# Kernel optimization log

Hardware: AMD Instinct MI355X
Metric: run time of the kernel (lower is better)

The kernel has to match this reference:

```python
import jax, jax.numpy as jnp
import numpy as np

B, T, F = 128, 64, 2048
N, H, C = 1024, 1024, 22  # neurons, hidden_size, num_classes


def setup_inputs() -> dict:
    key = jax.random.key(0)
    ks = jax.random.split(key, 9)
    def w(k, shape, fan_in):
        return jax.random.normal(k, shape, dtype=jnp.float32) / np.sqrt(fan_in)
    return {
        "x": jax.random.normal(ks[0], (B, T, F), dtype=jnp.float32),
        "W1": w(ks[1], (N, F), F),
        "b1": jnp.zeros((N,), jnp.float32),
        "W_ih": w(ks[2], (4 * H, N), N),
        "b_ih": jnp.zeros((4 * H,), jnp.float32),
        "W_hh": w(ks[3], (4 * H, H), H),
        "b_hh": jnp.zeros((4 * H,), jnp.float32),
        "Wc": w(ks[4], (C, H), H),
        "bc": jnp.zeros((C,), jnp.float32),
    }


def reference(x, W1, b1, W_ih, b_ih, W_hh, b_hh, Wc, bc):
    b, t, _ = x.shape
    h0 = jnp.zeros((b, H), x.dtype)
    c0 = jnp.zeros((b, H), x.dtype)
    # Precompute the input-side projections for every step (batched GEMMs):
    z = jax.nn.relu(jnp.einsum("btf,nf->btn", x, W1) + b1)        # [B,T,N]
    xg = jnp.einsum("btn,gn->btg", z, W_ih) + b_ih                 # [B,T,4H]

    def step(carry, xg_t):
        h, c = carry
        gates = xg_t + h @ W_hh.T + b_hh                           # [B,4H]
        i, f, g, o = jnp.split(gates, 4, axis=-1)                  # torch LSTMCell gate order
        c = jax.nn.sigmoid(f) * c + jax.nn.sigmoid(i) * jnp.tanh(g)
        h = jax.nn.sigmoid(o) * jnp.tanh(c)
        return (h, c), h

    _, hs = jax.lax.scan(step, (h0, c0), jnp.swapaxes(xg, 0, 1))    # hs: [T,B,H]
    scores = jnp.einsum("tbh,ch->tbc", hs, Wc) + bc                # [T,B,C]
    scores = jnp.swapaxes(scores, 0, 1).reshape(-1, Wc.shape[0])    # [B*T, C]
    return scores
```

## Files before the change

### kernel.cpp

```cpp
#include <hip/hip_runtime.h>
#include <hip/hip_bf16.h>

typedef short bf16x8 __attribute__((ext_vector_type(8)));
typedef float f32x4 __attribute__((ext_vector_type(4)));

#define B_ 128
#define T_ 64
#define F_ 2048
#define N_ 1024
#define H_ 1024
#define C_ 22

__device__ __forceinline__ ushort f2bf(float f) {
    union { float f; unsigned u; } v; v.f = f;
    unsigned u = v.u;
    unsigned r = (u + 0x7FFFu + ((u >> 16) & 1u)) >> 16;
    return (ushort)r;
}
__device__ __forceinline__ float bf2f(ushort h) {
    union { unsigned u; float f; } v; v.u = ((unsigned)h) << 16;
    return v.f;
}

__global__ __launch_bounds__(256) void cvt_f32_bf16(const float* __restrict__ in,
                                                    ushort* __restrict__ out, int n4) {
    int i = blockIdx.x * blockDim.x + threadIdx.x;
    if (i < n4) {
        float4 v = ((const float4*)in)[i];
        ushort4 o;
        o.x = f2bf(v.x); o.y = f2bf(v.y); o.z = f2bf(v.z); o.w = f2bf(v.w);
        ((ushort4*)out)[i] = o;
    }
}

__global__ __launch_bounds__(256) void cvt_wc(const float* __restrict__ Wc,
                                              ushort* __restrict__ Wcb) {
    int i = blockIdx.x * 256 + threadIdx.x;
    int row = i >> 10;
    Wcb[i] = (row < C_) ? f2bf(Wc[i]) : (ushort)0;
}

__device__ __forceinline__ void gload16(const void* g, void* l) {
    __builtin_amdgcn_global_load_lds(
        (const __attribute__((address_space(1))) unsigned int*)g,
        (__attribute__((address_space(3))) unsigned int*)l, 16, 0, 0);
}

template<int K, bool RELU>
__global__ __launch_bounds__(256) void gemm_bt(const ushort* __restrict__ A,
                                               const ushort* __restrict__ Bm,
                                               const float* __restrict__ bias1,
                                               const float* __restrict__ bias2,
                                               ushort* __restrict__ C,
                                               int Nt, int Nn) {
    __shared__ ushort sA[128 * 32];
    __shared__ ushort sB[128 * 32];
    const int tid = threadIdx.x;
    const int lane = tid & 63, wv = tid >> 6;
    const int tm = blockIdx.x / Nt, tn = blockIdx.x % Nt;
    const int wm = wv >> 1, wn = wv & 1;

    const ushort* gA = A + (size_t)(tm * 128 + (tid >> 2)) * K + (tid & 3) * 8;
    const ushort* gB = Bm + (size_t)(tn * 128 + (tid >> 2)) * K + (tid & 3) * 8;
    char* lAb = (char*)sA + wv * 1024;
    char* lBb = (char*)sB + wv * 1024;

    f32x4 acc[4][4] = {};

    for (int kt = 0; kt < K / 32; kt++) {
        const ushort* a0 = gA + kt * 32;
        const ushort* b0 = gB + kt * 32;
        gload16(a0, lAb);
        gload16(a0 + 64 * K, lAb + 4096);
        gload16(b0, lBb);
        gload16(b0 + 64 * K, lBb + 4096);
        __syncthreads();

        bf16x8 af[4], bfv[4];
#pragma unroll
        for (int i = 0; i < 4; i++)
            af[i] = *(const bf16x8*)&sA[(wm * 64 + i * 16 + (lane & 15)) * 32 + (lane >> 4) * 8];
#pragma unroll
        for (int j = 0; j < 4; j++)
            bfv[j] = *(const bf16x8*)&sB[(wn * 64 + j * 16 + (lane & 15)) * 32 + (lane >> 4) * 8];
#pragma unroll
        for (int i = 0; i < 4; i++)
#pragma unroll
            for (int j = 0; j < 4; j++)
                acc[i][j] = __builtin_amdgcn_mfma_f32_16x16x32_bf16(af[i], bfv[j], acc[i][j], 0, 0, 0);
        __syncthreads();
    }

#pragma unroll
    for (int j = 0; j < 4; j++) {
        int n = tn * 128 + wn * 64 + j * 16 + (lane & 15);
        float bias = bias1[n] + (bias2 ? bias2[n] : 0.f);
#pragma unroll
        for (int i = 0; i < 4; i++) {
            int mbase = tm * 128 + wm * 64 + i * 16 + (lane >> 4) * 4;
#pragma unroll
            for (int r = 0; r < 4; r++) {
                float v = acc[i][j][r] + bias;
                if (RELU) v = v > 0.f ? v : 0.f;
                C[(size_t)(mbase + r) * Nn + n] = f2bf(v);
            }
        }
    }
}

__global__ __launch_bounds__(256, 1) void lstm_persist(ushort* __restrict__ hs,
                                                       const ushort* __restrict__ xg,
                                                       const ushort* __restrict__ Whh,
                                                       unsigned* __restrict__ flags) {
    const int tid = threadIdx.x;
    const int lane = tid & 63;
    const int wv = tid >> 6;
    const int blk = (int)blockIdx.x;
    const int batch0 = (blk >> 6) * 32;
    const int hid0 = (blk & 63) * 16;
    const int gb = blk & ~63;

    bf16x8 breg[32];
    {
        const ushort* br = Whh + (size_t)(wv * H_ + hid0 + (lane & 15)) * H_ + ((lane >> 4) * 8);
#pragma unroll
        for (int ks = 0; ks < 32; ks++) breg[ks] = *(const bf16x8*)(br + ks * 32);
#pragma unroll
        for (int ks = 0; ks < 32; ks++) asm volatile("" : "+v"(breg[ks]));
    }

    __shared__ float lg[4][32][16];

    const int grow = tid >> 3;
    const int gjp = (tid & 7) * 2;
    float c0 = 0.f, c1 = 0.f;

    const int b = batch0 + grow;
    const int jj = hid0 + gjp;
    const ushort* xrow = xg + ((size_t)(b * T_) << 12) + jj;

    for (int t = 0; t < T_; t++) {
        const ushort* xr = xrow + ((size_t)t << 12);
        uint xi = *(const uint*)(xr);
        uint xf = *(const uint*)(xr + 1024);
        uint xgv = *(const uint*)(xr + 2048);
        uint xo = *(const uint*)(xr + 3072);

        const ushort* ar = hs + (size_t)t * (B_ * H_)
                         + (size_t)(batch0 + (lane & 15)) * H_ + ((lane >> 4) * 8);
        f32x4 acc0 = {}, acc1 = {};
#pragma unroll
        for (int ks = 0; ks < 32; ks++) {
            bf16x8 a0 = *(const bf16x8*)(ar + ks * 32);
            bf16x8 a1 = *(const bf16x8*)(ar + 16 * H_ + ks * 32);
            acc0 = __builtin_amdgcn_mfma_f32_16x16x32_bf16(a0, breg[ks], acc0, 0, 0, 0);
            acc1 = __builtin_amdgcn_mfma_f32_16x16x32_bf16(a1, breg[ks], acc1, 0, 0, 0);
        }
#pragma unroll
        for (int r = 0; r < 4; r++) {
            lg[wv][(lane >> 4) * 4 + r][lane & 15] = acc0[r];
            lg[wv][16 + (lane >> 4) * 4 + r][lane & 15] = acc1[r];
        }
        __syncthreads();

        {
            float pi0 = bf2f((ushort)(xi & 0xffff)) + lg[0][grow][gjp];
            float pi1 = bf2f((ushort)(xi >> 16)) + lg[0][grow][gjp + 1];
            float pf0 = bf2f((ushort)(xf & 0xffff)) + lg[1][grow][gjp];
            float pf1 = bf2f((ushort)(xf >> 16)) + lg[1][grow][gjp + 1];
            float pg0 = bf2f((ushort)(xgv & 0xffff)) + lg[2][grow][gjp];
            float pg1 = bf2f((ushort)(xgv >> 16)) + lg[2][grow][gjp + 1];
            float po0 = bf2f((ushort)(xo & 0xffff)) + lg[3][grow][gjp];
            float po1 = bf2f((ushort)(xo >> 16)) + lg[3][grow][gjp + 1];
            float si0 = 1.f / (1.f + expf(-pi0)), si1 = 1.f / (1.f + expf(-pi1));
            float sf0 = 1.f / (1.f + expf(-pf0)), sf1 = 1.f / (1.f + expf(-pf1));
            float tg0 = tanhf(pg0), tg1 = tanhf(pg1);
            float so0 = 1.f / (1.f + expf(-po0)), so1 = 1.f / (1.f + expf(-po1));
            c0 = sf0 * c0 + si0 * tg0;
            c1 = sf1 * c1 + si1 * tg1;
            uint hp = (uint)f2bf(so0 * tanhf(c0)) | ((uint)f2bf(so1 * tanhf(c1)) << 16);
            unsigned* hp32 = (unsigned*)(hs + (size_t)(t + 1) * (B_ * H_) + (size_t)b * H_ + jj);
            __hip_atomic_store(hp32, hp, __ATOMIC_RELAXED, __HIP_MEMORY_SCOPE_AGENT);
        }
        __syncthreads();

        if (t < T_ - 1) {
            if (tid == 0)
                __hip_atomic_store(&flags[blk], (unsigned)(t + 1),
                                   __ATOMIC_RELAXED, __HIP_MEMORY_SCOPE_AGENT);
            if (wv == 0) {
                asm volatile("s_waitcnt vmcnt(0)" ::: "memory");
                for (;;) {
                    unsigned f = __hip_atomic_load(&flags[gb + lane],
                                                   __ATOMIC_RELAXED, __HIP_MEMORY_SCOPE_AGENT);
                    if (__ballot(f < (unsigned)(t + 1)) == 0ull) break;
                }
            }
            __syncthreads();
        }
    }
}

__global__ __launch_bounds__(256) void scores_mfma(const ushort* __restrict__ hs,
                                                   const ushort* __restrict__ Wcb,
                                                   const float* __restrict__ bc,
                                                   float* __restrict__ out) {
    const int tid = threadIdx.x, lane = tid & 63, w = tid >> 6;
    const int r0 = blockIdx.x * 64 + w * 16;
    const int rr = r0 + (lane & 15);
    const int b = rr >> 6, t = rr & 63;
    const ushort* arow = hs + (size_t)(t + 1) * (B_ * H_) + (size_t)b * H_ + ((lane >> 4) * 8);
    const ushort* brow0 = Wcb + (size_t)(lane & 15) * H_ + ((lane >> 4) * 8);
    const ushort* brow1 = brow0 + 16 * H_;

    f32x4 acc0 = {}, acc1 = {};
#pragma unroll
    for (int ks = 0; ks < 32; ks++) {
        bf16x8 a  = *(const bf16x8*)(arow + ks * 32);
        bf16x8 p0 = *(const bf16x8*)(brow0 + ks * 32);
        bf16x8 p1 = *(const bf16x8*)(brow1 + ks * 32);
        acc0 = __builtin_amdgcn_mfma_f32_16x16x32_bf16(a, p0, acc0, 0, 0, 0);
        acc1 = __builtin_amdgcn_mfma_f32_16x16x32_bf16(a, p1, acc1, 0, 0, 0);
    }
#pragma unroll
    for (int nf = 0; nf < 2; nf++) {
        int c = nf * 16 + (lane & 15);
        if (c < C_) {
            float bias = bc[c];
            f32x4 acc = nf ? acc1 : acc0;
#pragma unroll
            for (int r = 0; r < 4; r++) {
                int row = r0 + (lane >> 4) * 4 + r;
                out[(size_t)row * C_ + c] = acc[r] + bias;
            }
        }
    }
}

extern "C" void kernel_launch(void* const* d_in, const int* in_sizes, int n_in,
                              void* d_out, int out_size, void* d_ws, size_t ws_size,
                              hipStream_t stream) {
    const float* x = (const float*)d_in[0];
    const float* W1 = (const float*)d_in[1];
    const float* b1 = (const float*)d_in[2];
    const float* W_ih = (const float*)d_in[3];
    const float* b_ih = (const float*)d_in[4];
    const float* W_hh = (const float*)d_in[5];
    const float* b_hh = (const float*)d_in[6];
    const float* Wc = (const float*)d_in[7];
    const float* bc = (const float*)d_in[8];
    float* out = (float*)d_out;

    char* ws = (char*)d_ws;
    ushort* Xb   = (ushort*)(ws);
    ushort* W1b  = (ushort*)(ws + 33554432);
    ushort* Wihb = (ushort*)(ws + 37748736);
    ushort* Whhb = (ushort*)(ws + 46137344);
    ushort* z    = (ushort*)(ws + 54525952);
    ushort* xg   = (ushort*)(ws + 71303168);
    ushort* hs   = (ushort*)(ws + 138412032);
    ushort* Wcb  = (ushort*)(ws + 155451392);
    unsigned* flags = (unsigned*)(ws + 155516928);

    hipMemsetAsync(hs, 0, (size_t)B_ * H_ * sizeof(ushort), stream);
    hipMemsetAsync(flags, 0, 256 * sizeof(unsigned), stream);

    cvt_f32_bf16<<<16384, 256, 0, stream>>>(x, Xb, 4194304);
    cvt_f32_bf16<<<2048, 256, 0, stream>>>(W1, W1b, 524288);
    cvt_f32_bf16<<<4096, 256, 0, stream>>>(W_ih, Wihb, 1048576);
    cvt_f32_bf16<<<4096, 256, 0, stream>>>(W_hh, Whhb, 1048576);
    cvt_wc<<<128, 256, 0, stream>>>(Wc, Wcb);

    gemm_bt<2048, true><<<512, 256, 0, stream>>>(Xb, W1b, b1, nullptr, z, 8, 1024);
    gemm_bt<1024, false><<<2048, 256, 0, stream>>>(z, Wihb, b_ih, b_hh, xg, 32, 4096);

    {
        void* hsv = (void*)hs; void* xgv = (void*)xg; void* whv = (void*)Whhb; void* flv = (void*)flags;
        void* args[] = { &hsv, &xgv, &whv, &flv };
        hipLaunchCooperativeKernel((void*)lstm_persist, dim3(256), dim3(256), args, 0, stream);
    }

    scores_mfma<<<128, 256, 0, stream>>>(hs, Wcb, bc, out);
}
```

Baseline: 829.0 us.

## Fuse input-to-hidden GEMM into persistent LSTM kernel with register-resident W_ih

Drops the separate z·W_ih^T GEMM and its large bf16 xg buffer. Each persistent block now also keeps its W_ih slice in registers and computes the input projection per step, issuing it before the inter-block flag wait so it overlaps the barrier. Transcendentals move to fast __expf-based sigmoid/tanh, and the cooperative launch becomes a normal launch. This doubles register pressure (64 bf16x8 weight vectors per thread), adds serial per-step MFMA work, and drops the co-residency guarantee that the spin-wait relies on.

After: 2.471 ms. 198% more time.

```diff
diff --git a/kernel.cpp b/kernel.cpp
--- a/kernel.cpp
+++ b/kernel.cpp
@@ -17,10 +17,8 @@
     unsigned r = (u + 0x7FFFu + ((u >> 16) & 1u)) >> 16;
     return (ushort)r;
 }
-__device__ __forceinline__ float bf2f(ushort h) {
-    union { unsigned u; float f; } v; v.u = ((unsigned)h) << 16;
-    return v.f;
-}
+__device__ __forceinline__ float sigm_f(float x) { return 1.f / (1.f + __expf(-x)); }
+__device__ __forceinline__ float tanh_f(float x) { return 1.f - 2.f / (1.f + __expf(2.f * x)); }
 
 __global__ __launch_bounds__(256) void cvt_f32_bf16(const float* __restrict__ in,
                                                     ushort* __restrict__ out, int n4) {
@@ -50,7 +48,6 @@
 __global__ __launch_bounds__(256) void gemm_bt(const ushort* __restrict__ A,
                                                const ushort* __restrict__ Bm,
                                                const float* __restrict__ bias1,
-                                               const float* __restrict__ bias2,
                                                ushort* __restrict__ C,
                                                int Nt, int Nn) {
     __shared__ ushort sA[128 * 32];
@@ -94,7 +91,7 @@
 #pragma unroll
     for (int j = 0; j < 4; j++) {
         int n = tn * 128 + wn * 64 + j * 16 + (lane & 15);
-        float bias = bias1[n] + (bias2 ? bias2[n] : 0.f);
+        float bias = bias1[n];
 #pragma unroll
         for (int i = 0; i < 4; i++) {
             int mbase = tm * 128 + wm * 64 + i * 16 + (lane >> 4) * 4;
@@ -108,10 +105,13 @@
     }
 }
 
-__global__ __launch_bounds__(256, 1) void lstm_persist(ushort* __restrict__ hs,
-                                                       const ushort* __restrict__ xg,
-                                                       const ushort* __restrict__ Whh,
-                                                       unsigned* __restrict__ flags) {
+__global__ __launch_bounds__(256, 1) void lstm_fused2(ushort* __restrict__ hs,
+                                                      const ushort* __restrict__ z,
+                                                      const ushort* __restrict__ Whh,
+                                                      const ushort* __restrict__ Wih,
+                                                      const float* __restrict__ b_ih,
+                                                      const float* __restrict__ b_hh,
+                                                      unsigned* __restrict__ flags) {
     const int tid = threadIdx.x;
     const int lane = tid & 63;
     const int wv = tid >> 6;
@@ -120,83 +120,100 @@
     const int hid0 = (blk & 63) * 16;
     const int gb = blk & ~63;
 
-    bf16x8 breg[32];
+    bf16x8 whh[32], wih[32];
     {
-        const ushort* br = Whh + (size_t)(wv * H_ + hid0 + (lane & 15)) * H_ + ((lane >> 4) * 8);
-#pragma unroll
-        for (int ks = 0; ks < 32; ks++) breg[ks] = *(const bf16x8*)(br + ks * 32);
-#pragma unroll
-        for (int ks = 0; ks < 32; ks++) asm volatile("" : "+v"(breg[ks]));
+        const size_t roff = (size_t)(wv * H_ + hid0 + (lane & 15)) * H_ + ((lane >> 4) * 8);
+        const ushort* brh = Whh + roff;
+        const ushort* bri = Wih + roff;
+#pragma unroll
+        for (int ks = 0; ks < 32; ks++) whh[ks] = *(const bf16x8*)(brh + ks * 32);
+#pragma unroll
+        for (int ks = 0; ks < 32; ks++) wih[ks] = *(const bf16x8*)(bri + ks * 32);
+#pragma unroll
+        for (int ks = 0; ks < 32; ks++) asm volatile("" : "+v"(whh[ks]));
+#pragma unroll
+        for (int ks = 0; ks < 32; ks++) asm volatile("" : "+v"(wih[ks]));
     }
 
     __shared__ float lg[4][32][16];
 
     const int grow = tid >> 3;
     const int gjp = (tid & 7) * 2;
-    float c0 = 0.f, c1 = 0.f;
-
     const int b = batch0 + grow;
     const int jj = hid0 + gjp;
-    const ushort* xrow = xg + ((size_t)(b * T_) << 12) + jj;
+    float bsum[8];
+#pragma unroll
+    for (int g = 0; g < 4; g++) {
+        bsum[g * 2]     = b_ih[g * H_ + jj]     + b_hh[g * H_ + jj];
+        bsum[g * 2 + 1] = b_ih[g * H_ + jj + 1] + b_hh[g * H_ + jj + 1];
+    }
+    float c0 = 0.f, c1 = 0.f;
+
+    const ushort* zbase = z + (size_t)(batch0 + (lane & 15)) * (T_ * N_) + ((lane >> 4) * 8);
 
     for (int t = 0; t < T_; t++) {
-        const ushort* xr = xrow + ((size_t)t << 12);
-        uint xi = *(const uint*)(xr);
-        uint xf = *(const uint*)(xr + 1024);
-        uint xgv = *(const uint*)(xr + 2048);
-        uint xo = *(const uint*)(xr + 3072);
-
-        const ushort* ar = hs + (size_t)t * (B_ * H_)
-                         + (size_t)(batch0 + (lane & 15)) * H_ + ((lane >> 4) * 8);
+        const ushort* zr = zbase + (size_t)t * N_;
         f32x4 acc0 = {}, acc1 = {};
 #pragma unroll
         for (int ks = 0; ks < 32; ks++) {
-            bf16x8 a0 = *(const bf16x8*)(ar + ks * 32);
-            bf16x8 a1 = *(const bf16x8*)(ar + 16 * H_ + ks * 32);
-            acc0 = __builtin_amdgcn_mfma_f32_16x16x32_bf16(a0, breg[ks], acc0, 0, 0, 0);
-            acc1 = __builtin_amdgcn_mfma_f32_16x16x32_bf16(a1, breg[ks], acc1, 0, 0, 0);
-        }
-#pragma unroll
-        for (int r = 0; r < 4; r++) {
-            lg[wv][(lane >> 4) * 4 + r][lane & 15] = acc0[r];
-            lg[wv][16 + (lane >> 4) * 4 + r][lane & 15] = acc1[r];
-        }
-        __syncthreads();
-
-        {
-            float pi0 = bf2f((ushort)(xi & 0xffff)) + lg[0][grow][gjp];
-            float pi1 = bf2f((ushort)(xi >> 16)) + lg[0][grow][gjp + 1];
-            float pf0 = bf2f((ushort)(xf & 0xffff)) + lg[1][grow][gjp];
-            float pf1 = bf2f((ushort)(xf >> 16)) + lg[1][grow][gjp + 1];
-            float pg0 = bf2f((ushort)(xgv & 0xffff)) + lg[2][grow][gjp];
-            float pg1 = bf2f((ushort)(xgv >> 16)) + lg[2][grow][gjp + 1];
-            float po0 = bf2f((ushort)(xo & 0xffff)) + lg[3][grow][gjp];
-            float po1 = bf2f((ushort)(xo >> 16)) + lg[3][grow][gjp + 1];
-            float si0 = 1.f / (1.f + expf(-pi0)), si1 = 1.f / (1.f + expf(-pi1));
-            float sf0 = 1.f / (1.f + expf(-pf0)), sf1 = 1.f / (1.f + expf(-pf1));
-            float tg0 = tanhf(pg0), tg1 = tanhf(pg1);
-            float so0 = 1.f / (1.f + expf(-po0)), so1 = 1.f / (1.f + expf(-po1));
-            c0 = sf0 * c0 + si0 * tg0;
-            c1 = sf1 * c1 + si1 * tg1;
-            uint hp = (uint)f2bf(so0 * tanhf(c0)) | ((uint)f2bf(so1 * tanhf(c1)) << 16);
-            unsigned* hp32 = (unsigned*)(hs + (size_t)(t + 1) * (B_ * H_) + (size_t)b * H_ + jj);
-            __hip_atomic_store(hp32, hp, __ATOMIC_RELAXED, __HIP_MEMORY_SCOPE_AGENT);
-        }
-        __syncthreads();
-
-        if (t < T_ - 1) {
-            if (tid == 0)
-                __hip_atomic_store(&flags[blk], (unsigned)(t + 1),
-                                   __ATOMIC_RELAXED, __HIP_MEMORY_SCOPE_AGENT);
+            bf16x8 a0 = *(const bf16x8*)(zr + ks * 32);
+            bf16x8 a1 = *(const bf16x8*)(zr + (size_t)16 * (T_ * N_) + ks * 32);
+            acc0 = __builtin_amdgcn_mfma_f32_16x16x32_bf16(a0, wih[ks], acc0, 0, 0, 0);
+            acc1 = __builtin_amdgcn_mfma_f32_16x16x32_bf16(a1, wih[ks], acc1, 0, 0, 0);
+        }
+
+        if (t > 0) {
             if (wv == 0) {
                 asm volatile("s_waitcnt vmcnt(0)" ::: "memory");
                 for (;;) {
                     unsigned f = __hip_atomic_load(&flags[gb + lane],
                                                    __ATOMIC_RELAXED, __HIP_MEMORY_SCOPE_AGENT);
-                    if (__ballot(f < (unsigned)(t + 1)) == 0ull) break;
+                    if (__ballot(f < (unsigned)t) == 0ull) break;
                 }
+                asm volatile("" ::: "memory");
             }
             __syncthreads();
+            __threadfence();
+        }
+
+        const ushort* ar = hs + (size_t)t * (B_ * H_)
+                         + (size_t)(batch0 + (lane & 15)) * H_ + ((lane >> 4) * 8);
+#pragma unroll
+        for (int ks = 0; ks < 32; ks++) {
+            bf16x8 a0 = *(const bf16x8*)(ar + ks * 32);
+            bf16x8 a1 = *(const bf16x8*)(ar + 16 * H_ + ks * 32);
+            acc0 = __builtin_amdgcn_mfma_f32_16x16x32_bf16(a0, whh[ks], acc0, 0, 0, 0);
+            acc1 = __builtin_amdgcn_mfma_f32_16x16x32_bf16(a1, whh[ks], acc1, 0, 0, 0);
+        }
+#pragma unroll
+        for (int r = 0; r < 4; r++) {
+            lg[wv][(lane >> 4) * 4 + r][lane & 15] = acc0[r];
+            lg[wv][16 + (lane >> 4) * 4 + r][lane & 15] = acc1[r];
+        }
+        __syncthreads();
+
+        {
+            float pi0 = lg[0][grow][gjp]     + bsum[0];
+            float pi1 = lg[0][grow][gjp + 1] + bsum[1];
+            float pf0 = lg[1][grow][gjp]     + bsum[2];
+            float pf1 = lg[1][grow][gjp + 1] + bsum[3];
+            float pg0 = lg[2][grow][gjp]     + bsum[4];
+            float pg1 = lg[2][grow][gjp + 1] + bsum[5];
+            float po0 = lg[3][grow][gjp]     + bsum[6];
+            float po1 = lg[3][grow][gjp + 1] + bsum[7];
+            c0 = sigm_f(pf0) * c0 + sigm_f(pi0) * tanh_f(pg0);
+            c1 = sigm_f(pf1) * c1 + sigm_f(pi1) * tanh_f(pg1);
+            uint hp = (uint)f2bf(sigm_f(po0) * tanh_f(c0)) |
+                      ((uint)f2bf(sigm_f(po1) * tanh_f(c1)) << 16);
+            unsigned* hp32 = (unsigned*)(hs + (size_t)(t + 1) * (B_ * H_) + (size_t)b * H_ + jj);
+            __hip_atomic_store(hp32, hp, __ATOMIC_RELAXED, __HIP_MEMORY_SCOPE_AGENT);
+        }
+        __syncthreads();
+
+        if (tid == 0) {
+            __threadfence();
+            __hip_atomic_store(&flags[blk], (unsigned)(t + 1),
+                               __ATOMIC_RELAXED, __HIP_MEMORY_SCOPE_AGENT);
         }
     }
 }
@@ -257,10 +274,9 @@
     ushort* Wihb = (ushort*)(ws + 37748736);
     ushort* Whhb = (ushort*)(ws + 46137344);
     ushort* z    = (ushort*)(ws + 54525952);
-    ushort* xg   = (ushort*)(ws + 71303168);
-    ushort* hs   = (ushort*)(ws + 138412032);
-    ushort* Wcb  = (ushort*)(ws + 155451392);
-    unsigned* flags = (unsigned*)(ws + 155516928);
+    ushort* hs   = (ushort*)(ws + 71303168);
+    ushort* Wcb  = (ushort*)(ws + 88342528);
+    unsigned* flags = (unsigned*)(ws + 88408064);
 
     hipMemsetAsync(hs, 0, (size_t)B_ * H_ * sizeof(ushort), stream);
     hipMemsetAsync(flags, 0, 256 * sizeof(unsigned), stream);
@@ -271,14 +287,9 @@
     cvt_f32_bf16<<<4096, 256, 0, stream>>>(W_hh, Whhb, 1048576);
     cvt_wc<<<128, 256, 0, stream>>>(Wc, Wcb);
 
-    gemm_bt<2048, true><<<512, 256, 0, stream>>>(Xb, W1b, b1, nullptr, z, 8, 1024);
-    gemm_bt<1024, false><<<2048, 256, 0, stream>>>(z, Wihb, b_ih, b_hh, xg, 32, 4096);
-
-    {
-        void* hsv = (void*)hs; void* xgv = (void*)xg; void* whv = (void*)Whhb; void* flv = (void*)flags;
-        void* args[] = { &hsv, &xgv, &whv, &flv };
-        hipLaunchCooperativeKernel((void*)lstm_persist, dim3(256), dim3(256), args, 0, stream);
-    }
+    gemm_bt<2048, true><<<512, 256, 0, stream>>>(Xb, W1b, b1, z, 8, 1024);
+
+    lstm_fused2<<<256, 256, 0, stream>>>(hs, z, Whhb, Wihb, b_ih, b_hh, flags);
 
     scores_mfma<<<128, 256, 0, stream>>>(hs, Wcb, bc, out);
 }
```

## Prefetch next-step gate inputs, move flag wait to loop top, fast activations

Applied to the files above, without the earlier changes.

The persistent LSTM kernel now prefetches the next timestep's xg gate inputs before the recurrent MFMA loop, so that global load latency overlaps with compute. The inter-block flag wait moves to the top of each step and the explicit vmcnt wait before polling is removed. The accurate expf/tanhf calls are replaced with __expf-based sigmoid and tanh. The launch changes from hipLaunchCooperativeKernel to a plain launch. These trims per-step latency on the serial critical path, but co-residency of all 256 blocks is no longer guaranteed, and dropping the vmcnt wait before publishing the flag risks a memory-ordering race on hs.

Result: slower. 1.178 ms (+42.1%).

```diff
diff --git a/kernel.cpp b/kernel.cpp
--- a/kernel.cpp
+++ b/kernel.cpp
@@ -21,6 +21,8 @@
     union { unsigned u; float f; } v; v.u = ((unsigned)h) << 16;
     return v.f;
 }
+__device__ __forceinline__ float sigm_f(float x) { return 1.f / (1.f + __expf(-x)); }
+__device__ __forceinline__ float tanh_f(float x) { return 1.f - 2.f / (1.f + __expf(2.f * x)); }
 
 __global__ __launch_bounds__(256) void cvt_f32_bf16(const float* __restrict__ in,
                                                     ushort* __restrict__ out, int n4) {
@@ -108,10 +110,10 @@
     }
 }
 
-__global__ __launch_bounds__(256, 1) void lstm_persist(ushort* __restrict__ hs,
-                                                       const ushort* __restrict__ xg,
-                                                       const ushort* __restrict__ Whh,
-                                                       unsigned* __restrict__ flags) {
+__global__ __launch_bounds__(256, 1) void lstm_rec(ushort* __restrict__ hs,
+                                                   const ushort* __restrict__ xg,
+                                                   const ushort* __restrict__ Whh,
+                                                   unsigned* __restrict__ flags) {
     const int tid = threadIdx.x;
     const int lane = tid & 63;
     const int wv = tid >> 6;
@@ -120,31 +122,52 @@
     const int hid0 = (blk & 63) * 16;
     const int gb = blk & ~63;
 
-    bf16x8 breg[32];
+    bf16x8 whh[32];
     {
         const ushort* br = Whh + (size_t)(wv * H_ + hid0 + (lane & 15)) * H_ + ((lane >> 4) * 8);
 #pragma unroll
-        for (int ks = 0; ks < 32; ks++) breg[ks] = *(const bf16x8*)(br + ks * 32);
-#pragma unroll
-        for (int ks = 0; ks < 32; ks++) asm volatile("" : "+v"(breg[ks]));
+        for (int ks = 0; ks < 32; ks++)
+            asm volatile("global_load_dwordx4 %0, %1, off"
+                         : "=&v"(whh[ks]) : "v"(br + ks * 32) : "memory");
+        asm volatile("s_waitcnt vmcnt(0)" ::: "memory");
     }
 
     __shared__ float lg[4][32][16];
 
     const int grow = tid >> 3;
     const int gjp = (tid & 7) * 2;
-    float c0 = 0.f, c1 = 0.f;
-
     const int b = batch0 + grow;
     const int jj = hid0 + gjp;
     const ushort* xrow = xg + ((size_t)(b * T_) << 12) + jj;
 
+    float c0 = 0.f, c1 = 0.f;
+
+    uint xi = *(const uint*)(xrow);
+    uint xf = *(const uint*)(xrow + 1024);
+    uint xgv = *(const uint*)(xrow + 2048);
+    uint xo = *(const uint*)(xrow + 3072);
+
     for (int t = 0; t < T_; t++) {
-        const ushort* xr = xrow + ((size_t)t << 12);
-        uint xi = *(const uint*)(xr);
-        uint xf = *(const uint*)(xr + 1024);
-        uint xgv = *(const uint*)(xr + 2048);
-        uint xo = *(const uint*)(xr + 3072);
+        if (t > 0) {
+            if (wv == 0) {
+                for (;;) {
+                    unsigned f = __hip_atomic_load(&flags[gb + lane],
+                                                   __ATOMIC_RELAXED, __HIP_MEMORY_SCOPE_AGENT);
+                    if (__ballot(f < (unsigned)t) == 0ull) break;
+                }
+                asm volatile("" ::: "memory");
+            }
+            __syncthreads();
+        }
+
+        uint ni = 0, nf2 = 0, ng = 0, no = 0;
+        if (t + 1 < T_) {
+            const ushort* xr = xrow + ((size_t)(t + 1) << 12);
+            ni  = *(const uint*)(xr);
+            nf2 = *(const uint*)(xr + 1024);
+            ng  = *(const uint*)(xr + 2048);
+            no  = *(const uint*)(xr + 3072);
+        }
 
         const ushort* ar = hs + (size_t)t * (B_ * H_)
                          + (size_t)(batch0 + (lane & 15)) * H_ + ((lane >> 4) * 8);
@@ -153,8 +176,8 @@
         for (int ks = 0; ks < 32; ks++) {
             bf16x8 a0 = *(const bf16x8*)(ar + ks * 32);
             bf16x8 a1 = *(const bf16x8*)(ar + 16 * H_ + ks * 32);
-            acc0 = __builtin_amdgcn_mfma_f32_16x16x32_bf16(a0, breg[ks], acc0, 0, 0, 0);
-            acc1 = __builtin_amdgcn_mfma_f32_16x16x32_bf16(a1, breg[ks], acc1, 0, 0, 0);
+            acc0 = __builtin_amdgcn_mfma_f32_16x16x32_bf16(a0, whh[ks], acc0, 0, 0, 0);
+            acc1 = __builtin_amdgcn_mfma_f32_16x16x32_bf16(a1, whh[ks], acc1, 0, 0, 0);
         }
 #pragma unroll
         for (int r = 0; r < 4; r++) {
@@ -164,40 +187,28 @@
         __syncthreads();
 
         {
-            float pi0 = bf2f((ushort)(xi & 0xffff)) + lg[0][grow][gjp];
-            float pi1 = bf2f((ushort)(xi >> 16)) + lg[0][grow][gjp + 1];
-            float pf0 = bf2f((ushort)(xf & 0xffff)) + lg[1][grow][gjp];
-            float pf1 = bf2f((ushort)(xf >> 16)) + lg[1][grow][gjp + 1];
+            float pi0 = bf2f((ushort)(xi & 0xffff))  + lg[0][grow][gjp];
+            float pi1 = bf2f((ushort)(xi >> 16))     + lg[0][grow][gjp + 1];
+            float pf0 = bf2f((ushort)(xf & 0xffff))  + lg[1][grow][gjp];
+            float pf1 = bf2f((ushort)(xf >> 16))     + lg[1][grow][gjp + 1];
             float pg0 = bf2f((ushort)(xgv & 0xffff)) + lg[2][grow][gjp];
-            float pg1 = bf2f((ushort)(xgv >> 16)) + lg[2][grow][gjp + 1];
-            float po0 = bf2f((ushort)(xo & 0xffff)) + lg[3][grow][gjp];
-            float po1 = bf2f((ushort)(xo >> 16)) + lg[3][grow][gjp + 1];
-            float si0 = 1.f / (1.f + expf(-pi0)), si1 = 1.f / (1.f + expf(-pi1));
-            float sf0 = 1.f / (1.f + expf(-pf0)), sf1 = 1.f / (1.f + expf(-pf1));
-            float tg0 = tanhf(pg0), tg1 = tanhf(pg1);
-            float so0 = 1.f / (1.f + expf(-po0)), so1 = 1.f / (1.f + expf(-po1));
-            c0 = sf0 * c0 + si0 * tg0;
-            c1 = sf1 * c1 + si1 * tg1;
-            uint hp = (uint)f2bf(so0 * tanhf(c0)) | ((uint)f2bf(so1 * tanhf(c1)) << 16);
+            float pg1 = bf2f((ushort)(xgv >> 16))    + lg[2][grow][gjp + 1];
+            float po0 = bf2f((ushort)(xo & 0xffff))  + lg[3][grow][gjp];
+            float po1 = bf2f((ushort)(xo >> 16))     + lg[3][grow][gjp + 1];
+            c0 = sigm_f(pf0) * c0 + sigm_f(pi0) * tanh_f(pg0);
+            c1 = sigm_f(pf1) * c1 + sigm_f(pi1) * tanh_f(pg1);
+            uint hp = (uint)f2bf(sigm_f(po0) * tanh_f(c0)) |
+                      ((uint)f2bf(sigm_f(po1) * tanh_f(c1)) << 16);
             unsigned* hp32 = (unsigned*)(hs + (size_t)(t + 1) * (B_ * H_) + (size_t)b * H_ + jj);
             __hip_atomic_store(hp32, hp, __ATOMIC_RELAXED, __HIP_MEMORY_SCOPE_AGENT);
         }
         __syncthreads();
 
-        if (t < T_ - 1) {
-            if (tid == 0)
-                __hip_atomic_store(&flags[blk], (unsigned)(t + 1),
-                                   __ATOMIC_RELAXED, __HIP_MEMORY_SCOPE_AGENT);
-            if (wv == 0) {
-                asm volatile("s_waitcnt vmcnt(0)" ::: "memory");
-                for (;;) {
-                    unsigned f = __hip_atomic_load(&flags[gb + lane],
-                                                   __ATOMIC_RELAXED, __HIP_MEMORY_SCOPE_AGENT);
-                    if (__ballot(f < (unsigned)(t + 1)) == 0ull) break;
-                }
-            }
-            __syncthreads();
-        }
+        if (tid == 0)
+            __hip_atomic_store(&flags[blk], (unsigned)(t + 1),
+                               __ATOMIC_RELAXED, __HIP_MEMORY_SCOPE_AGENT);
+
+        xi = ni; xf = nf2; xgv = ng; xo = no;
     }
 }
 
@@ -274,11 +285,7 @@
     gemm_bt<2048, true><<<512, 256, 0, stream>>>(Xb, W1b, b1, nullptr, z, 8, 1024);
     gemm_bt<1024, false><<<2048, 256, 0, stream>>>(z, Wihb, b_ih, b_hh, xg, 32, 4096);
 
-    {
-        void* hsv = (void*)hs; void* xgv = (void*)xg; void* whv = (void*)Whhb; void* flv = (void*)flags;
-        void* args[] = { &hsv, &xgv, &whv, &flv };
-        hipLaunchCooperativeKernel((void*)lstm_persist, dim3(256), dim3(256), args, 0, stream);
-    }
+    lstm_rec<<<256, 256, 0, stream>>>(hs, xg, Whhb, flags);
 
     scores_mfma<<<128, 256, 0, stream>>>(hs, Wcb, bc, out);
 }
```
